# Optimization experiments

Measured on AMD Instinct MI355X. Metric: run time of the kernel, lower is better.

Reference implementation:

```python
import jax, jax.numpy as jnp
import numpy as np

N = 50000   # function nodes
E = 100000  # edges per relation
H = 8       # heads
D = 96      # per-head dim (768 // 8)
L = 2       # conv layers
B = 256     # graphs in batch
C = 31      # num_classes + 1


def setup_inputs() -> dict:
    key = jax.random.key(0)
    ks = jax.random.split(key, 24)
    s = 0.05  # weight init scale to keep attention logits sane
    inp = {
        "function_feats": jax.random.normal(ks[0], (N, 768), jnp.float32),
        "w_src_calls": jax.random.normal(ks[1], (L, 768, 768), jnp.float32) * s,
        "b_src_calls": jnp.zeros((L, 768), jnp.float32),
        "w_dst_calls": jax.random.normal(ks[2], (L, 768, 768), jnp.float32) * s,
        "b_dst_calls": jnp.zeros((L, 768), jnp.float32),
        "attn_calls": jax.random.normal(ks[3], (L, H, D), jnp.float32) * s,
        "w_src_cb": jax.random.normal(ks[4], (L, 768, 768), jnp.float32) * s,
        "b_src_cb": jnp.zeros((L, 768), jnp.float32),
        "w_dst_cb": jax.random.normal(ks[5], (L, 768, 768), jnp.float32) * s,
        "b_dst_cb": jnp.zeros((L, 768), jnp.float32),
        "attn_cb": jax.random.normal(ks[6], (L, H, D), jnp.float32) * s,
        "fc1_w": jax.random.normal(ks[7], (768, 256), jnp.float32) * s,
        "fc1_b": jnp.zeros((256,), jnp.float32),
        "fc2_w": jax.random.normal(ks[8], (256, C), jnp.float32) * s,
        "fc2_b": jnp.zeros((C,), jnp.float32),
        "calls_src": jax.random.randint(ks[9], (E,), 0, N),
        "calls_dst": jax.random.randint(ks[10], (E,), 0, N),
        "cb_src": jax.random.randint(ks[11], (E,), 0, N),
        "cb_dst": jax.random.randint(ks[12], (E,), 0, N),
        "graph_start_idx": jnp.sort(jax.random.randint(ks[13], (B,), 0, N)),
        "labels": jax.random.randint(ks[14], (B,), 0, C),
    }
    return inp


def _gatv2(h, Ws, bs, Wd, bd, attn, src, dst):
    # DGL GATv2Conv: e_ij = attn . leaky_relu(W_src h_i + W_dst h_j); softmax over in-edges of j
    fs = (h @ Ws + bs).reshape(N, H, D)
    fd = (h @ Wd + bd).reshape(N, H, D)
    e = jax.nn.leaky_relu(fs[src] + fd[dst], negative_slope=0.2)  # [E,H,D]
    score = jnp.einsum('ehd,hd->eh', e, attn)                      # [E,H]
    mx = jax.ops.segment_max(score, dst, num_segments=N)           # [N,H]
    ex = jnp.exp(score - mx[dst])
    den = jax.ops.segment_sum(ex, dst, num_segments=N)
    alpha = ex / den[dst]                                          # edge softmax
    return jax.ops.segment_sum(fs[src] * alpha[..., None], dst, num_segments=N)  # [N,H,D]


def reference(function_feats, w_src_calls, b_src_calls, w_dst_calls, b_dst_calls,
              attn_calls, w_src_cb, b_src_cb, w_dst_cb, b_dst_cb, attn_cb,
              fc1_w, fc1_b, fc2_w, fc2_b,
              calls_src, calls_dst, cb_src, cb_dst, graph_start_idx, labels):
    h = function_feats
    for l in range(L):
        o = _gatv2(h, w_src_calls[l], b_src_calls[l], w_dst_calls[l], b_dst_calls[l],
                   attn_calls[l], calls_src, calls_dst)
        o = o + _gatv2(h, w_src_cb[l], b_src_cb[l], w_dst_cb[l], b_dst_cb[l],
                       attn_cb[l], cb_src, cb_dst)  # HeteroGraphConv 'sum' aggregate
        h = o.reshape(N, H * D) + h                  # residual
    func_embed = h[graph_start_idx]                  # [B,768] gather first node per graph
    logits = jax.nn.relu(func_embed @ fc1_w + fc1_b) @ fc2_w + fc2_b  # [B,C]
    logp = jax.nn.log_softmax(logits, axis=-1)
    loss = -jnp.mean(jnp.take_along_axis(logp, labels[:, None], axis=1))
    return (loss, logits)
```

## Files before the change

kernel.cpp:

```cpp
#include <hip/hip_runtime.h>
#include <hip/hip_bf16.h>
#include <math.h>

#define N_NODES 50000
#define NE      100000
#define FDIM    768
#define NFUSE   3072
#define NB      256
#define NC      31

#define A1_CAP  16384
#define N1_CAP  4096
#define EB      ((NE + 255) / 256)
#define SCT     (2 * EB)
#define GTN     12

#define TWT_BLOCKS  (8 * 576)
#define BIAS_BLOCKS 24
#define CVT_BLOCKS  512
#define SETUP_BLOCKS (TWT_BLOCKS + BIAS_BLOCKS + CVT_BLOCKS)
#define SETUPH_BLOCKS (SETUP_BLOCKS + SCT)

typedef __hip_bfloat16 bf16;
typedef __attribute__((ext_vector_type(8))) short bf16x8;
typedef __attribute__((ext_vector_type(4))) float f32x4;

__device__ inline float u2f(unsigned short u) { return __uint_as_float(((unsigned int)u) << 16); }
__device__ inline unsigned short f2u(float f) { return __bfloat16_as_ushort(__float2bfloat16(f)); }

__device__ inline float aload_f(const float* p) {
    return __hip_atomic_load(p, __ATOMIC_RELAXED, __HIP_MEMORY_SCOPE_AGENT);
}
__device__ inline void astore_f(float* p, float v) {
    __hip_atomic_store(p, v, __ATOMIC_RELAXED, __HIP_MEMORY_SCOPE_AGENT);
}

__device__ inline void load_lds16(const void* g, void* l) {
    __builtin_amdgcn_global_load_lds(
        (const __attribute__((address_space(1))) void*)g,
        (__attribute__((address_space(3))) void*)l, 16, 0, 0);
}

__global__ __launch_bounds__(256) void markA_kernel(const int* __restrict__ gsi,
                                                    const int* __restrict__ src0,
                                                    const int* __restrict__ dst0,
                                                    const int* __restrict__ src1,
                                                    const int* __restrict__ dst1,
                                                    int* __restrict__ fL1,
                                                    int* __restrict__ fA1,
                                                    int* __restrict__ list1, int* __restrict__ idx1,
                                                    int* __restrict__ list2, int* __restrict__ idx2,
                                                    int* __restrict__ list0,
                                                    int* __restrict__ cnts) {
    const int t = threadIdx.x, b = blockIdx.x;
    if (b == 0) {
        const int n = gsi[t];
        if (atomicExch(&fL1[n], 1) == 0) {
            const int p = atomicAdd(&cnts[1], 1);
            if (p < N1_CAP) { list2[p] = n; idx2[n] = p; } else idx2[n] = 0;
        }
        if (atomicExch(&fA1[n], 1) == 0) {
            const int p = atomicAdd(&cnts[0], 1);
            if (p < A1_CAP) { list1[p] = n; idx1[n] = p; } else idx1[n] = 0;
        }
        const bool first = (t == 0) || (gsi[t - 1] != n);
        if (first) {
            const int p = atomicAdd(&cnts[2], 1);
            if (p < 256) list0[p] = n;
        }
        return;
    }
    __shared__ int g[256];
    g[t] = gsi[t];
    __syncthreads();
    const int eb = b - 1;
    const int r = (eb >= EB) ? 1 : 0;
    const int e = (eb - r * EB) * 256 + t;
    if (e >= NE) return;
    const int d = (r ? dst1 : dst0)[e];
    int lo = 0, hi = 256;
    while (lo < hi) { const int mid = (lo + hi) >> 1; if (g[mid] < d) lo = mid + 1; else hi = mid; }
    if (lo < 256 && g[lo] == d) {
        const int s = (r ? src1 : src0)[e];
        if (atomicExch(&fL1[s], 1) == 0) {
            const int p = atomicAdd(&cnts[1], 1);
            if (p < N1_CAP) { list2[p] = s; idx2[s] = p; } else idx2[s] = 0;
        }
        if (atomicExch(&fA1[s], 1) == 0) {
            const int p = atomicAdd(&cnts[0], 1);
            if (p < A1_CAP) { list1[p] = s; idx1[s] = p; } else idx1[s] = 0;
        }
    }
}

__global__ __launch_bounds__(256) void markB_kernel(const int* __restrict__ src0,
                                                    const int* __restrict__ dst0,
                                                    const int* __restrict__ src1,
                                                    const int* __restrict__ dst1,
                                                    const int* __restrict__ fL1,
                                                    int* __restrict__ fA1,
                                                    int* __restrict__ list1, int* __restrict__ idx1,
                                                    int* __restrict__ cnts) {
    const int e = blockIdx.x * 256 + threadIdx.x;
    if (e >= NE) return;
    const int r = blockIdx.y;
    if (fL1[(r ? dst1 : dst0)[e]]) {
        const int s = (r ? src1 : src0)[e];
        if (atomicExch(&fA1[s], 1) == 0) {
            const int p = atomicAdd(&cnts[0], 1);
            if (p < A1_CAP) { list1[p] = s; idx1[s] = p; } else idx1[s] = 0;
        }
    }
}

__global__ __launch_bounds__(256) void setup_kernel(const float* __restrict__ w_sc,
                                                    const float* __restrict__ w_dc,
                                                    const float* __restrict__ w_scb,
                                                    const float* __restrict__ w_dcb,
                                                    const float* __restrict__ b_sc,
                                                    const float* __restrict__ b_dc,
                                                    const float* __restrict__ b_scb,
                                                    const float* __restrict__ b_dcb,
                                                    const float* __restrict__ feats,
                                                    const int* __restrict__ list,
                                                    const int* __restrict__ pcnt,
                                                    bf16* __restrict__ WtFl,
                                                    float* __restrict__ pb,
                                                    bf16* __restrict__ h,
                                                    const int* __restrict__ dst0,
                                                    const int* __restrict__ dst1,
                                                    const int* __restrict__ fL1,
                                                    const int* __restrict__ idx2,
                                                    int* __restrict__ dega) {
    __shared__ float tile[32][33];
    const int b = blockIdx.x;
    const int t = threadIdx.x;
    if (b < TWT_BLOCKS) {
        const int z = b / 576, cell = b % 576;
        const int l = z >> 2, sel2 = z & 3;
        const float* src;
        if (sel2 == 0) src = w_sc; else if (sel2 == 1) src = w_scb;
        else if (sel2 == 2) src = w_dc; else src = w_dcb;
        src += (size_t)l * FDIM * FDIM;
        bf16* dst = WtFl + (size_t)z * FDIM * FDIM;
        const int tx = t & 31, ty = t >> 5;
        const int x0 = (cell % 24) * 32, y0 = (cell / 24) * 32;
#pragma unroll
        for (int q = 0; q < 4; ++q)
            tile[ty + q * 8][tx] = src[(size_t)(y0 + ty + q * 8) * FDIM + x0 + tx];
        __syncthreads();
#pragma unroll
        for (int q = 0; q < 4; ++q)
            dst[(size_t)(x0 + ty + q * 8) * FDIM + y0 + tx] = __float2bfloat16(tile[tx][ty + q * 8]);
    } else if (b < TWT_BLOCKS + BIAS_BLOCKS) {
        const int idx = (b - TWT_BLOCKS) * 256 + t;
        const int l = idx / NFUSE, c = idx % NFUSE;
        const int sel2 = c / FDIM, off = c % FDIM;
        const float* src;
        if (sel2 == 0) src = b_sc; else if (sel2 == 1) src = b_scb;
        else if (sel2 == 2) src = b_dc; else src = b_dcb;
        pb[idx] = src[l * FDIM + off];
    } else if (b < SETUP_BLOCKS) {
        int c = *pcnt; if (c > A1_CAP) c = A1_CAP;
        for (int i = b - TWT_BLOCKS - BIAS_BLOCKS; i < c; i += CVT_BLOCKS) {
            const int n = list[i];
            const float* s = feats + (size_t)n * FDIM;
            bf16* d = h + (size_t)n * FDIM;
            for (int k = t; k < FDIM; k += 256) d[k] = __float2bfloat16(s[k]);
        }
    } else {
        const int eb = b - SETUP_BLOCKS;
        const int r = (eb >= EB) ? 1 : 0;
        const int e = (eb - r * EB) * 256 + t;
        if (e < NE) {
            const int d = (r ? dst1 : dst0)[e];
            if (fL1[d]) atomicAdd(&dega[r * N1_CAP + idx2[d]], 1);
        }
    }
}

__global__ __launch_bounds__(256) void scana_kernel(const int* __restrict__ dega,
                                                    int* __restrict__ rowpa,
                                                    int* __restrict__ cursora) {
    __shared__ int part[256];
    const int t = threadIdx.x;
    for (int r = 0; r < 2; ++r) {
        const int base = r * N1_CAP;
        int loc[16];
        int s = 0;
#pragma unroll
        for (int q = 0; q < 16; ++q) { loc[q] = dega[base + t * 16 + q]; s += loc[q]; }
        part[t] = s;
        __syncthreads();
        for (int o = 1; o < 256; o <<= 1) {
            int x = (t >= o) ? part[t - o] : 0;
            __syncthreads();
            part[t] += x;
            __syncthreads();
        }
        int run = part[t] - s;
        const int rbase = r * (N1_CAP + 1);
#pragma unroll
        for (int q = 0; q < 16; ++q) {
            rowpa[rbase + t * 16 + q] = run;
            cursora[base + t * 16 + q] = run;
            run += loc[q];
        }
        if (t == 255) rowpa[rbase + N1_CAP] = run;
        __syncthreads();
    }
}

__global__ __launch_bounds__(256) void gemm2(const bf16* __restrict__ A,
                                             const bf16* __restrict__ Wt,
                                             const float* __restrict__ pb,
                                             bf16* __restrict__ C,
                                             const int* __restrict__ rlA,
                                             const int* __restrict__ cntAp, int capA,
                                             const int* __restrict__ rlB,
                                             const int* __restrict__ cntBp, int capB,
                                             const int* __restrict__ idxmap,
                                             int blocksA,
                                             int sct,
                                             const int* __restrict__ dst0,
                                             const int* __restrict__ dst1,
                                             const int* __restrict__ fL1,
                                             const int* __restrict__ idx2,
                                             int* __restrict__ cursora,
                                             int* __restrict__ eida) {
    int bid = blockIdx.x;
    if (bid < sct) {
        const int r = (bid >= EB) ? 1 : 0;
        const int e = (bid - r * EB) * 256 + threadIdx.x;
        if (e < NE) {
            const int d = (r ? dst1 : dst0)[e];
            if (fL1[d]) {
                const int p = atomicAdd(&cursora[r * N1_CAP + idx2[d]], 1);
                eida[(size_t)r * NE + p] = e;
            }
        }
        return;
    }
    bid -= sct;
    const int* rowlist;
    int cnt, col0;
    if (bid < blocksA) {
        rowlist = rlA; cnt = *cntAp; if (cnt > capA) cnt = capA; col0 = 0;
    } else {
        bid -= blocksA;
        rowlist = rlB; cnt = *cntBp; if (cnt > capB) cnt = capB; col0 = 1536;
    }
    const int tm = bid / GTN, tn = bid % GTN;
    const int m0 = tm * 128, n0 = tn * 128;
    if (m0 >= cnt) return;

    __shared__ __align__(16) short Abuf[128 * 64];
    __shared__ __align__(16) short Bbuf[128 * 64];
    const int t = threadIdx.x;
    const int wid = t >> 6, lane = t & 63;
    const int wr = wid >> 1, wc = wid & 1;
    const int lr = lane & 15, lk = lane >> 4;

    const f32x4 zero4 = {0.f, 0.f, 0.f, 0.f};
    f32x4 acc[4][4];
#pragma unroll
    for (int i = 0; i < 4; ++i)
#pragma unroll
        for (int j = 0; j < 4; ++j) acc[i][j] = zero4;

    int arow[4], brow[4], acol[4], ldsoff[4];
#pragma unroll
    for (int i = 0; i < 4; ++i) {
        const int s = i * 256 + t;
        const int rr = s >> 3, pch = s & 7;
        int ri = m0 + rr; if (ri >= cnt) ri = cnt - 1;
        arow[i] = rowlist[ri];
        brow[i] = col0 + n0 + rr;
        acol[i] = (pch ^ (rr & 7)) << 3;
        ldsoff[i] = (i * 256 + wid * 64) * 16;
    }

    for (int kt = 0; kt < FDIM / 64; ++kt) {
        const int k0 = kt * 64;
#pragma unroll
        for (int i = 0; i < 4; ++i) {
            load_lds16(A + (size_t)arow[i] * FDIM + k0 + acol[i], (char*)Abuf + ldsoff[i]);
            load_lds16(Wt + (size_t)brow[i] * FDIM + k0 + acol[i], (char*)Bbuf + ldsoff[i]);
        }
        __syncthreads();
#pragma unroll
        for (int kh = 0; kh < 2; ++kh) {
            bf16x8 av[4], bv[4];
            const int c = kh * 4 + lk;
#pragma unroll
            for (int i = 0; i < 4; ++i) {
                const int mm = wr * 64 + i * 16 + lr;
                av[i] = *(const bf16x8*)((const char*)Abuf + mm * 128 + ((c ^ (mm & 7)) << 4));
            }
#pragma unroll
            for (int j = 0; j < 4; ++j) {
                const int nn = wc * 64 + j * 16 + lr;
                bv[j] = *(const bf16x8*)((const char*)Bbuf + nn * 128 + ((c ^ (nn & 7)) << 4));
            }
#pragma unroll
            for (int i = 0; i < 4; ++i)
#pragma unroll
                for (int j = 0; j < 4; ++j)
                    acc[i][j] = __builtin_amdgcn_mfma_f32_16x16x32_bf16(bv[j], av[i], acc[i][j], 0, 0, 0);
        }
        __syncthreads();
    }

#pragma unroll
    for (int i = 0; i < 4; ++i) {
        const int row = m0 + wr * 64 + i * 16 + lr;
        if (row < cnt) {
            const int crow = idxmap[rowlist[row]];
#pragma unroll
            for (int j = 0; j < 4; ++j) {
                const int col = col0 + n0 + wc * 64 + j * 16 + lk * 4;
                const float4 b4 = *(const float4*)(pb + col);
                ushort4 w;
                w.x = f2u(acc[i][j][0] + b4.x);
                w.y = f2u(acc[i][j][1] + b4.y);
                w.z = f2u(acc[i][j][2] + b4.z);
                w.w = f2u(acc[i][j][3] + b4.w);
                *(ushort4*)(C + (size_t)crow * NFUSE + col) = w;
            }
        }
    }
}

__device__ inline void att_accum(const bf16* __restrict__ fsd, const int* __restrict__ idxsrc,
                                 int fdrow, int lane, const float* __restrict__ attn,
                                 int beg, int end,
                                 const int* __restrict__ eid, const int* __restrict__ src,
                                 int fs_off, int fd_off, float* __restrict__ out) {
    float fdv[12], atv[12];
    {
        const ushort4* pfd = (const ushort4*)(fsd + (size_t)fdrow * NFUSE + fd_off + lane * 12);
        const ushort4 d0 = pfd[0], d1 = pfd[1], d2 = pfd[2];
        fdv[0] = u2f(d0.x); fdv[1] = u2f(d0.y); fdv[2] = u2f(d0.z); fdv[3] = u2f(d0.w);
        fdv[4] = u2f(d1.x); fdv[5] = u2f(d1.y); fdv[6] = u2f(d1.z); fdv[7] = u2f(d1.w);
        fdv[8] = u2f(d2.x); fdv[9] = u2f(d2.y); fdv[10] = u2f(d2.z); fdv[11] = u2f(d2.w);
        const float4* pat = (const float4*)(attn + lane * 12);
        const float4 a0 = pat[0], a1 = pat[1], a2 = pat[2];
        atv[0] = a0.x; atv[1] = a0.y; atv[2] = a0.z; atv[3] = a0.w;
        atv[4] = a1.x; atv[5] = a1.y; atv[6] = a1.z; atv[7] = a1.w;
        atv[8] = a2.x; atv[9] = a2.y; atv[10] = a2.z; atv[11] = a2.w;
    }
    float m = -INFINITY, den = 0.f;
    float acc[12];
#pragma unroll
    for (int j = 0; j < 12; ++j) acc[j] = 0.f;

    for (int i = beg; i < end; ++i) {
        const int e = eid[i];
        const ushort4* pf = (const ushort4*)(fsd + (size_t)idxsrc[src[e]] * NFUSE + fs_off + lane * 12);
        const ushort4 a0 = pf[0], a1 = pf[1], a2 = pf[2];
        float fsv[12];
        fsv[0] = u2f(a0.x); fsv[1] = u2f(a0.y); fsv[2] = u2f(a0.z); fsv[3] = u2f(a0.w);
        fsv[4] = u2f(a1.x); fsv[5] = u2f(a1.y); fsv[6] = u2f(a1.z); fsv[7] = u2f(a1.w);
        fsv[8] = u2f(a2.x); fsv[9] = u2f(a2.y); fsv[10] = u2f(a2.z); fsv[11] = u2f(a2.w);
        float p = 0.f;
#pragma unroll
        for (int j = 0; j < 12; ++j) {
            float x = fsv[j] + fdv[j];
            x = (x > 0.f) ? x : 0.2f * x;
            p += x * atv[j];
        }
        p += __shfl_xor(p, 1);
        p += __shfl_xor(p, 2);
        p += __shfl_xor(p, 4);
        if (p > m) {
            const float sc = expf(m - p);
            den *= sc;
#pragma unroll
            for (int j = 0; j < 12; ++j) acc[j] *= sc;
            m = p;
        }
        const float w = expf(p - m);
        den += w;
#pragma unroll
        for (int j = 0; j < 12; ++j) acc[j] += w * fsv[j];
    }
    const float inv = (den > 0.f) ? 1.f / den : 0.f;
#pragma unroll
    for (int j = 0; j < 12; ++j) out[j] = acc[j] * inv;
}

__global__ __launch_bounds__(256) void aggL_kernel(const bf16* __restrict__ fsd,
                                                   const int* __restrict__ idx1,
                                                   const float* __restrict__ attn0,
                                                   const float* __restrict__ attn1,
                                                   const int* __restrict__ rowpa,
                                                   const int* __restrict__ eida,
                                                   const int* __restrict__ src0,
                                                   const int* __restrict__ src1,
                                                   bf16* __restrict__ h,
                                                   const int* __restrict__ list2,
                                                   const int* __restrict__ pcnt) {
    const int wid = threadIdx.x >> 6;
    const int lane = threadIdx.x & 63;
    int cnt = *pcnt; if (cnt > N1_CAP) cnt = N1_CAP;
    const int i = blockIdx.x * 4 + wid;
    if (i >= cnt) return;
    const int n = list2[i];
    const int fdrow = idx1[n];

    float a0[12], a1[12];
    att_accum(fsd, idx1, fdrow, lane, attn0, rowpa[i], rowpa[i + 1],
              eida, src0, 0, 1536, a0);
    att_accum(fsd, idx1, fdrow, lane, attn1, rowpa[(N1_CAP + 1) + i], rowpa[(N1_CAP + 1) + i + 1],
              eida + NE, src1, 768, 2304, a1);

    const size_t base = (size_t)n * FDIM + lane * 12;
    const ushort4* ph = (const ushort4*)(h + base);
    const ushort4 h0 = ph[0], h1 = ph[1], h2 = ph[2];
    ushort4 r0, r1, r2;
    r0.x = f2u(u2f(h0.x) + a0[0] + a1[0]);  r0.y = f2u(u2f(h0.y) + a0[1] + a1[1]);
    r0.z = f2u(u2f(h0.z) + a0[2] + a1[2]);  r0.w = f2u(u2f(h0.w) + a0[3] + a1[3]);
    r1.x = f2u(u2f(h1.x) + a0[4] + a1[4]);  r1.y = f2u(u2f(h1.y) + a0[5] + a1[5]);
    r1.z = f2u(u2f(h1.z) + a0[6] + a1[6]);  r1.w = f2u(u2f(h1.w) + a0[7] + a1[7]);
    r2.x = f2u(u2f(h2.x) + a0[8] + a1[8]);  r2.y = f2u(u2f(h2.y) + a0[9] + a1[9]);
    r2.z = f2u(u2f(h2.z) + a0[10] + a1[10]); r2.w = f2u(u2f(h2.w) + a0[11] + a1[11]);
    ((ushort4*)(h + base))[0] = r0; ((ushort4*)(h + base))[1] = r1; ((ushort4*)(h + base))[2] = r2;
}

__global__ __launch_bounds__(256) void agghead_kernel(const bf16* __restrict__ fsd,
                                                      const int* __restrict__ idx2,
                                                      const float* __restrict__ attn0,
                                                      const float* __restrict__ attn1,
                                                      const int* __restrict__ rowpa,
                                                      const int* __restrict__ eida,
                                                      const int* __restrict__ src0,
                                                      const int* __restrict__ src1,
                                                      const bf16* __restrict__ h,
                                                      const int* __restrict__ gsi,
                                                      const float* __restrict__ fc1w,
                                                      const float* __restrict__ fc1b,
                                                      const float* __restrict__ fc2w,
                                                      const float* __restrict__ fc2b,
                                                      const int* __restrict__ labels,
                                                      int* __restrict__ cnts,
                                                      float* __restrict__ out) {
    __shared__ float a0s[FDIM], a1s[FDIM], fe[FDIM];
    __shared__ float hid[256];
    const int b = blockIdx.x, t = threadIdx.x;
    const int n = gsi[b];
    const int wv = t >> 6, lane = t & 63;
    if (wv < 2) {
        const int j = idx2[n];
        const int rb = wv * (N1_CAP + 1);
        float v[12];
        att_accum(fsd, idx2, j, lane, wv ? attn1 : attn0,
                  rowpa[rb + j], rowpa[rb + j + 1],
                  eida + (size_t)wv * NE, wv ? src1 : src0,
                  wv ? 768 : 0, wv ? 2304 : 1536, v);
        float* dl = wv ? a1s : a0s;
#pragma unroll
        for (int q = 0; q < 12; ++q) dl[lane * 12 + q] = v[q];
    }
    __syncthreads();
    for (int d = t; d < FDIM; d += 256)
        fe[d] = u2f(__bfloat16_as_ushort(h[(size_t)n * FDIM + d])) + a0s[d] + a1s[d];
    __syncthreads();
    float acc = fc1b[t];
    for (int k = 0; k < FDIM; ++k) acc += fe[k] * fc1w[k * 256 + t];
    hid[t] = (acc > 0.f) ? acc : 0.f;
    __syncthreads();
    if (t < NC) {
        float a2 = fc2b[t];
        for (int k = 0; k < 256; ++k) a2 += hid[k] * fc2w[k * NC + t];
        astore_f(&out[1 + b * NC + t], a2);
    }

    __syncthreads();
    __shared__ int amlast;
    if (t == 0) amlast = (atomicAdd(&cnts[9], 1) == NB - 1) ? 1 : 0;
    __syncthreads();
    if (amlast) {
        __shared__ float red[256];
        float m = -INFINITY;
        float lg[NC];
#pragma unroll
        for (int c = 0; c < NC; ++c) {
            lg[c] = aload_f(&out[1 + t * NC + c]);
            m = fmaxf(m, lg[c]);
        }
        float sum = 0.f;
#pragma unroll
        for (int c = 0; c < NC; ++c) sum += expf(lg[c] - m);
        const float lse = m + logf(sum);
        const float ll = lg[labels[t]];
        red[t] = lse - ll;
        __syncthreads();
        for (int s = 128; s > 0; s >>= 1) {
            if (t < s) red[t] += red[t + s];
            __syncthreads();
        }
        if (t == 0) out[0] = red[0] / (float)NB;
    }
}

extern "C" void kernel_launch(void* const* d_in, const int* in_sizes, int n_in,
                              void* d_out, int out_size, void* d_ws, size_t ws_size,
                              hipStream_t stream) {
    const float* feats = (const float*)d_in[0];
    const int* src0    = (const int*)d_in[15];
    const int* dst0    = (const int*)d_in[16];
    const int* src1    = (const int*)d_in[17];
    const int* dst1    = (const int*)d_in[18];
    const int* gsi     = (const int*)d_in[19];
    const int* labels  = (const int*)d_in[20];

    const size_t NF = (size_t)N_NODES * FDIM;
    const size_t WSZ = (size_t)FDIM * FDIM;
    char* p = (char*)d_ws;
    bf16* h    = (bf16*)p;  p += NF * 2;
    bf16* fsd  = (bf16*)p;  p += (size_t)A1_CAP * NFUSE * 2;
    bf16* WtFl = (bf16*)p;  p += 8 * WSZ * 2;
    float* pb  = (float*)p; p += 2 * NFUSE * 4;
    int* fA1  = (int*)p;    p += (size_t)N_NODES * 4;
    int* fL1  = (int*)p;    p += (size_t)N_NODES * 4;
    int* cnts = (int*)p;    p += 64 * 4;
    int* dega = (int*)p;    p += 2 * (size_t)N1_CAP * 4;
    const size_t zero_bytes = (2 * (size_t)N_NODES + 64 + 2 * (size_t)N1_CAP) * 4;
    int* idx1  = (int*)p;   p += (size_t)N_NODES * 4;
    int* idx2  = (int*)p;   p += (size_t)N_NODES * 4;
    int* list1 = (int*)p;   p += (size_t)A1_CAP * 4;
    int* list2 = (int*)p;   p += (size_t)N1_CAP * 4;
    int* list0 = (int*)p;   p += 256 * 4;
    int* rowpa = (int*)p;   p += 2 * ((size_t)N1_CAP + 1) * 4;
    int* cursora = (int*)p; p += 2 * (size_t)N1_CAP * 4;
    int* eida  = (int*)p;   p += 2 * (size_t)NE * 4;

    hipMemsetAsync(fA1, 0, zero_bytes, stream);
    markA_kernel<<<1 + SCT, 256, 0, stream>>>(gsi, src0, dst0, src1, dst1,
                                              fL1, fA1, list1, idx1, list2, idx2, list0, cnts);
    markB_kernel<<<dim3(EB, 2), 256, 0, stream>>>(src0, dst0, src1, dst1, fL1, fA1,
                                                  list1, idx1, cnts);
    setup_kernel<<<SETUPH_BLOCKS, 256, 0, stream>>>(
        (const float*)d_in[1], (const float*)d_in[3], (const float*)d_in[6], (const float*)d_in[8],
        (const float*)d_in[2], (const float*)d_in[4], (const float*)d_in[7], (const float*)d_in[9],
        feats, list1, &cnts[0], WtFl, pb, h, dst0, dst1, fL1, idx2, dega);
    scana_kernel<<<1, 256, 0, stream>>>(dega, rowpa, cursora);

    const int blocksA0 = (A1_CAP / 128) * GTN;
    const int blocksB0 = (N1_CAP / 128) * GTN;
    const int blocksA1 = (N1_CAP / 128) * GTN;
    const int blocksB1 = (256 / 128) * GTN;

    gemm2<<<SCT + blocksA0 + blocksB0, 256, 0, stream>>>(
        h, WtFl, pb, fsd,
        list1, &cnts[0], A1_CAP, list2, &cnts[1], N1_CAP, idx1, blocksA0,
        SCT, dst0, dst1, fL1, idx2, cursora, eida);
    aggL_kernel<<<(N1_CAP + 3) / 4, 256, 0, stream>>>(
        fsd, idx1, (const float*)d_in[5], (const float*)d_in[10],
        rowpa, eida, src0, src1, h, list2, &cnts[1]);
    gemm2<<<blocksA1 + blocksB1, 256, 0, stream>>>(
        h, WtFl + 4 * WSZ, pb + NFUSE, fsd,
        list2, &cnts[1], N1_CAP, list0, &cnts[2], 256, idx2, blocksA1,
        0, dst0, dst1, fL1, idx2, cursora, eida);
    agghead_kernel<<<NB, 256, 0, stream>>>(
        fsd, idx2, (const float*)d_in[5] + FDIM, (const float*)d_in[10] + FDIM,
        rowpa, eida, src0, src1, h, gsi,
        (const float*)d_in[11], (const float*)d_in[12],
        (const float*)d_in[13], (const float*)d_in[14],
        labels, cnts, (float*)d_out);
}
```

Before: 189.5 us.

## Split frontier marking from compaction and move edge scatter out of GEMM

Marking kernels now only set flag bits with plain stores, and a separate compact kernel builds the node lists and index maps in node order with one atomic per selected node. The edge scatter that was folded into the first GEMM launch becomes its own kernel, and the memset is replaced by a small zeroing kernel. The aim is to cut atomic contention from repeated atomicExch/atomicAdd on duplicate sources and keep the GEMM launch uniform. The cost is extra kernel launches (zero, compact, scatter) and an additional full pass over the node flags.

Result: faster. 163.1 us (-14.0%).

```diff
diff --git a/kernel.cpp b/kernel.cpp
--- a/kernel.cpp
+++ b/kernel.cpp
@@ -11,6 +11,7 @@
 
 #define A1_CAP  16384
 #define N1_CAP  4096
+#define NBLK    ((N_NODES + 255) / 256)
 #define EB      ((NE + 255) / 256)
 #define SCT     (2 * EB)
 #define GTN     12
@@ -21,6 +22,8 @@
 #define SETUP_BLOCKS (TWT_BLOCKS + BIAS_BLOCKS + CVT_BLOCKS)
 #define SETUPH_BLOCKS (SETUP_BLOCKS + SCT)
 
+#define ZERO_INTS (2 * N_NODES + 64 + 2 * N1_CAP)
+
 typedef __hip_bfloat16 bf16;
 typedef __attribute__((ext_vector_type(8))) short bf16x8;
 typedef __attribute__((ext_vector_type(4))) float f32x4;
@@ -39,6 +42,12 @@
     __builtin_amdgcn_global_load_lds(
         (const __attribute__((address_space(1))) void*)g,
         (__attribute__((address_space(3))) void*)l, 16, 0, 0);
+}
+
+__global__ __launch_bounds__(256) void zero_kernel(int4* __restrict__ dst) {
+    const int i = blockIdx.x * 256 + threadIdx.x;
+    const int n4 = (ZERO_INTS + 3) / 4;
+    if (i < n4) dst[i] = make_int4(0, 0, 0, 0);
 }
 
 __global__ __launch_bounds__(256) void markA_kernel(const int* __restrict__ gsi,
@@ -48,21 +57,12 @@
                                                     const int* __restrict__ dst1,
                                                     int* __restrict__ fL1,
                                                     int* __restrict__ fA1,
-                                                    int* __restrict__ list1, int* __restrict__ idx1,
-                                                    int* __restrict__ list2, int* __restrict__ idx2,
                                                     int* __restrict__ list0,
                                                     int* __restrict__ cnts) {
     const int t = threadIdx.x, b = blockIdx.x;
     if (b == 0) {
         const int n = gsi[t];
-        if (atomicExch(&fL1[n], 1) == 0) {
-            const int p = atomicAdd(&cnts[1], 1);
-            if (p < N1_CAP) { list2[p] = n; idx2[n] = p; } else idx2[n] = 0;
-        }
-        if (atomicExch(&fA1[n], 1) == 0) {
-            const int p = atomicAdd(&cnts[0], 1);
-            if (p < A1_CAP) { list1[p] = n; idx1[n] = p; } else idx1[n] = 0;
-        }
+        fL1[n] = 1; fA1[n] = 1;
         const bool first = (t == 0) || (gsi[t - 1] != n);
         if (first) {
             const int p = atomicAdd(&cnts[2], 1);
@@ -82,14 +82,7 @@
     while (lo < hi) { const int mid = (lo + hi) >> 1; if (g[mid] < d) lo = mid + 1; else hi = mid; }
     if (lo < 256 && g[lo] == d) {
         const int s = (r ? src1 : src0)[e];
-        if (atomicExch(&fL1[s], 1) == 0) {
-            const int p = atomicAdd(&cnts[1], 1);
-            if (p < N1_CAP) { list2[p] = s; idx2[s] = p; } else idx2[s] = 0;
-        }
-        if (atomicExch(&fA1[s], 1) == 0) {
-            const int p = atomicAdd(&cnts[0], 1);
-            if (p < A1_CAP) { list1[p] = s; idx1[s] = p; } else idx1[s] = 0;
-        }
+        fL1[s] = 1; fA1[s] = 1;
     }
 }
 
@@ -98,18 +91,27 @@
                                                     const int* __restrict__ src1,
                                                     const int* __restrict__ dst1,
                                                     const int* __restrict__ fL1,
-                                                    int* __restrict__ fA1,
-                                                    int* __restrict__ list1, int* __restrict__ idx1,
-                                                    int* __restrict__ cnts) {
+                                                    int* __restrict__ fA1) {
     const int e = blockIdx.x * 256 + threadIdx.x;
     if (e >= NE) return;
     const int r = blockIdx.y;
-    if (fL1[(r ? dst1 : dst0)[e]]) {
-        const int s = (r ? src1 : src0)[e];
-        if (atomicExch(&fA1[s], 1) == 0) {
-            const int p = atomicAdd(&cnts[0], 1);
-            if (p < A1_CAP) { list1[p] = s; idx1[s] = p; } else idx1[s] = 0;
-        }
+    if (fL1[(r ? dst1 : dst0)[e]]) fA1[(r ? src1 : src0)[e]] = 1;
+}
+
+__global__ __launch_bounds__(256) void compact_kernel(const int* __restrict__ fA1,
+                                                      const int* __restrict__ fL1,
+                                                      int* __restrict__ list1, int* __restrict__ idx1,
+                                                      int* __restrict__ list2, int* __restrict__ idx2,
+                                                      int* __restrict__ cnts) {
+    const int n = blockIdx.x * 256 + threadIdx.x;
+    if (n >= N_NODES) return;
+    if (fA1[n]) {
+        const int p = atomicAdd(&cnts[0], 1);
+        if (p < A1_CAP) { list1[p] = n; idx1[n] = p; } else idx1[n] = 0;
+    }
+    if (fL1[n]) {
+        const int p = atomicAdd(&cnts[1], 1);
+        if (p < N1_CAP) { list2[p] = n; idx2[n] = p; } else idx2[n] = 0;
     }
 }
 
@@ -211,6 +213,22 @@
     }
 }
 
+__global__ __launch_bounds__(256) void scattera_kernel(const int* __restrict__ dst0,
+                                                       const int* __restrict__ dst1,
+                                                       const int* __restrict__ fL1,
+                                                       const int* __restrict__ idx2,
+                                                       int* __restrict__ cursora,
+                                                       int* __restrict__ eida) {
+    const int e = blockIdx.x * 256 + threadIdx.x;
+    if (e >= NE) return;
+    const int r = blockIdx.y;
+    const int d = (r ? dst1 : dst0)[e];
+    if (fL1[d]) {
+        const int p = atomicAdd(&cursora[r * N1_CAP + idx2[d]], 1);
+        eida[(size_t)r * NE + p] = e;
+    }
+}
+
 __global__ __launch_bounds__(256) void gemm2(const bf16* __restrict__ A,
                                              const bf16* __restrict__ Wt,
                                              const float* __restrict__ pb,
@@ -220,28 +238,8 @@
                                              const int* __restrict__ rlB,
                                              const int* __restrict__ cntBp, int capB,
                                              const int* __restrict__ idxmap,
-                                             int blocksA,
-                                             int sct,
-                                             const int* __restrict__ dst0,
-                                             const int* __restrict__ dst1,
-                                             const int* __restrict__ fL1,
-                                             const int* __restrict__ idx2,
-                                             int* __restrict__ cursora,
-                                             int* __restrict__ eida) {
+                                             int blocksA) {
     int bid = blockIdx.x;
-    if (bid < sct) {
-        const int r = (bid >= EB) ? 1 : 0;
-        const int e = (bid - r * EB) * 256 + threadIdx.x;
-        if (e < NE) {
-            const int d = (r ? dst1 : dst0)[e];
-            if (fL1[d]) {
-                const int p = atomicAdd(&cursora[r * N1_CAP + idx2[d]], 1);
-                eida[(size_t)r * NE + p] = e;
-            }
-        }
-        return;
-    }
-    bid -= sct;
     const int* rowlist;
     int cnt, col0;
     if (bid < blocksA) {
@@ -525,7 +523,6 @@
     int* fL1  = (int*)p;    p += (size_t)N_NODES * 4;
     int* cnts = (int*)p;    p += 64 * 4;
     int* dega = (int*)p;    p += 2 * (size_t)N1_CAP * 4;
-    const size_t zero_bytes = (2 * (size_t)N_NODES + 64 + 2 * (size_t)N1_CAP) * 4;
     int* idx1  = (int*)p;   p += (size_t)N_NODES * 4;
     int* idx2  = (int*)p;   p += (size_t)N_NODES * 4;
     int* list1 = (int*)p;   p += (size_t)A1_CAP * 4;
@@ -535,33 +532,32 @@
     int* cursora = (int*)p; p += 2 * (size_t)N1_CAP * 4;
     int* eida  = (int*)p;   p += 2 * (size_t)NE * 4;
 
-    hipMemsetAsync(fA1, 0, zero_bytes, stream);
+    zero_kernel<<<(ZERO_INTS / 4 + 255) / 256, 256, 0, stream>>>((int4*)fA1);
     markA_kernel<<<1 + SCT, 256, 0, stream>>>(gsi, src0, dst0, src1, dst1,
-                                              fL1, fA1, list1, idx1, list2, idx2, list0, cnts);
-    markB_kernel<<<dim3(EB, 2), 256, 0, stream>>>(src0, dst0, src1, dst1, fL1, fA1,
-                                                  list1, idx1, cnts);
+                                              fL1, fA1, list0, cnts);
+    markB_kernel<<<dim3(EB, 2), 256, 0, stream>>>(src0, dst0, src1, dst1, fL1, fA1);
+    compact_kernel<<<NBLK, 256, 0, stream>>>(fA1, fL1, list1, idx1, list2, idx2, cnts);
     setup_kernel<<<SETUPH_BLOCKS, 256, 0, stream>>>(
         (const float*)d_in[1], (const float*)d_in[3], (const float*)d_in[6], (const float*)d_in[8],
         (const float*)d_in[2], (const float*)d_in[4], (const float*)d_in[7], (const float*)d_in[9],
         feats, list1, &cnts[0], WtFl, pb, h, dst0, dst1, fL1, idx2, dega);
     scana_kernel<<<1, 256, 0, stream>>>(dega, rowpa, cursora);
+    scattera_kernel<<<dim3(EB, 2), 256, 0, stream>>>(dst0, dst1, fL1, idx2, cursora, eida);
 
     const int blocksA0 = (A1_CAP / 128) * GTN;
     const int blocksB0 = (N1_CAP / 128) * GTN;
     const int blocksA1 = (N1_CAP / 128) * GTN;
     const int blocksB1 = (256 / 128) * GTN;
 
-    gemm2<<<SCT + blocksA0 + blocksB0, 256, 0, stream>>>(
+    gemm2<<<blocksA0 + blocksB0, 256, 0, stream>>>(
         h, WtFl, pb, fsd,
-        list1, &cnts[0], A1_CAP, list2, &cnts[1], N1_CAP, idx1, blocksA0,
-        SCT, dst0, dst1, fL1, idx2, cursora, eida);
+        list1, &cnts[0], A1_CAP, list2, &cnts[1], N1_CAP, idx1, blocksA0);
     aggL_kernel<<<(N1_CAP + 3) / 4, 256, 0, stream>>>(
         fsd, idx1, (const float*)d_in[5], (const float*)d_in[10],
         rowpa, eida, src0, src1, h, list2, &cnts[1]);
     gemm2<<<blocksA1 + blocksB1, 256, 0, stream>>>(
         h, WtFl + 4 * WSZ, pb + NFUSE, fsd,
-        list2, &cnts[1], N1_CAP, list0, &cnts[2], 256, idx2, blocksA1,
-        0, dst0, dst1, fL1, idx2, cursora, eida);
+        list2, &cnts[1], N1_CAP, list0, &cnts[2], 256, idx2, blocksA1);
     agghead_kernel<<<NB, 256, 0, stream>>>(
         fsd, idx2, (const float*)d_in[5] + FDIM, (const float*)d_in[10] + FDIM,
         rowpa, eida, src0, src1, h, gsi,
```
